# Performance work log

Hardware: AMD Instinct MI355X
Metric: run time of the kernel (lower is better)

## Reference

```python
import jax, jax.numpy as jnp
import numpy as np
from jax import lax

V, D, H = 32000, 512, 512  # vocab, embedding_dim, hidden_size (must match for the DxD matmul chain)
B, T, A = 64, 256, 4       # batch, sentence len, aspect len
EPS = 1e-5


def setup_inputs() -> dict:
    key = jax.random.key(0)
    ks = jax.random.split(key, 12)
    sc = 0.05
    return {
        "x": jax.random.randint(ks[0], (B, T), 0, V),
        "s": jax.random.randint(ks[1], (B, A), 0, V),
        "embed": jax.random.normal(ks[2], (V, D), jnp.float32) * sc,
        "W_ih": jax.random.normal(ks[3], (4 * H, D), jnp.float32) * sc,
        "W_hh": jax.random.normal(ks[4], (4 * H, H), jnp.float32) * sc,
        "b_lstm": jax.random.normal(ks[5], (4 * H,), jnp.float32) * sc,
        "w_y": jax.random.normal(ks[6], (D, D), jnp.float32) * sc,
        "w_t": jax.random.normal(ks[7], (D, D), jnp.float32) * sc,
        "w_p": jax.random.normal(ks[8], (D, D), jnp.float32) * sc,
        "w_x": jax.random.normal(ks[9], (D, D), jnp.float32) * sc,
        "w_f": jax.random.normal(ks[10], (D, D), jnp.float32) * sc,
        "b_f": jax.random.normal(ks[11], (D,), jnp.float32) * sc,
    }


def _lstm(emb, W_ih, W_hh, b):
    # emb: [B, T, D] -> hidden states [B, T, H]; PyTorch gate order i,f,g,o
    Bx = emb.shape[0]
    Hh = W_hh.shape[1]
    h0 = jnp.zeros((Bx, Hh), emb.dtype)
    c0 = jnp.zeros((Bx, Hh), emb.dtype)

    def step(carry, x_t):
        h, c = carry
        z = x_t @ W_ih.T + h @ W_hh.T + b  # [B, 4H]
        i, f, g, o = jnp.split(z, 4, axis=-1)
        c = jax.nn.sigmoid(f) * c + jax.nn.sigmoid(i) * jnp.tanh(g)
        h = jax.nn.sigmoid(o) * jnp.tanh(c)
        return (h, c), h

    _, hs = lax.scan(step, (h0, c0), jnp.swapaxes(emb, 0, 1))
    return jnp.swapaxes(hs, 0, 1)  # [B, T, H]


def reference(x, s, embed, W_ih, W_hh, b_lstm, w_y, w_t, w_p, w_x, w_f, b_f):
    # 1) embed + LSTM over the sentence
    emb = embed[x]                      # [B, T, D]
    Hs = _lstm(emb, W_ih, W_hh, b_lstm)  # [B, T, H]

    # 2) aspect: embed, batch-normalize per feature, sum over aspect tokens
    s_emb = embed[s]                    # [B, A, D]
    mu = s_emb.mean(axis=(0, 1))
    var = s_emb.var(axis=(0, 1))
    s_norm = ((s_emb - mu) * lax.rsqrt(var + EPS)).sum(axis=1)  # [B, D]

    # 3) FFT circular correlation: m_t = ifft(fft(h_t) * conj(fft(s))).real
    Hf = jnp.fft.fft(Hs, axis=-1)                      # [B, T, D] complex
    Sf = jnp.conj(jnp.fft.fft(s_norm, axis=-1))        # [B, D]
    m = jnp.fft.ifft(Hf * Sf[:, None, :], axis=-1).real.astype(Hs.dtype)  # [B, T, D]

    # 4) attention chain
    Y = jnp.tanh(jnp.einsum('de,bte->btd', w_y, m))            # [B, T, D]
    alpha = jax.nn.softmax(jnp.einsum('de,bte->btd', w_t, Y), axis=1)  # softmax over time
    r = jnp.einsum('btd,btd->bd', alpha, Hs)                   # [B, D]
    h_star = jnp.tanh(r @ w_p.T + Hs[:, -1] @ w_x.T)           # [B, D]
    return jax.nn.softmax(h_star @ w_f.T + b_f, axis=-1)       # [B, D]
```

## Files before the change

kernel.cpp:

```cpp
#include <hip/hip_runtime.h>


typedef __bf16 bf16x8 __attribute__((ext_vector_type(8)));
typedef float f32x4 __attribute__((ext_vector_type(4)));

#define B_ 64
#define T_ 256
#define D_ 512
#define H4 2048

__device__ __forceinline__ unsigned short f2bf(float f) {
    unsigned u = __float_as_uint(f);
    u += 0x7fffu + ((u >> 16) & 1u);
    return (unsigned short)(u >> 16);
}
__device__ __forceinline__ float bf2f(unsigned short x) {
    return __uint_as_float(((unsigned)x) << 16);
}
__device__ __forceinline__ float bf2f_lo(unsigned u) { return __uint_as_float(u << 16); }
__device__ __forceinline__ float bf2f_hi(unsigned u) { return __uint_as_float(u & 0xffff0000u); }

__device__ __forceinline__ float frcp(float x) { return __builtin_amdgcn_rcpf(x); }
__device__ __forceinline__ float fast_sigmoid(float x) {
    return frcp(1.f + __expf(-x));
}
__device__ __forceinline__ float fast_tanh(float x) {
    return 1.f - 2.f * frcp(1.f + __expf(2.f * x));
}

__global__ __launch_bounds__(256)
void gemm_bt(const void* __restrict__ Abase, int a_f32,
             const int* __restrict__ gather_idx,
             const float* __restrict__ Bmat,
             const float* __restrict__ circ_src,
             const float* __restrict__ bias,
             unsigned short* __restrict__ outb,
             float* __restrict__ outf,
             int N, int K,
             long A_bstride, long out_bstride,
             int act)
{
    __shared__ __align__(16) unsigned short Asm[128 * 40];
    __shared__ __align__(16) unsigned short Bsm[128 * 40];

    const int bz = blockIdx.z;
    const int tile_n = blockIdx.x * 128;
    const int tile_m = blockIdx.y * 128;
    const int tid = threadIdx.x;
    const int lane = tid & 63;
    const int w = tid >> 6;
    const int wm = (w >> 1) * 64;
    const int wn = (w & 1) * 64;

    const int srow = tid >> 1;
    const int skc = (tid & 1) * 16;

    const float* arow_f = nullptr;
    const unsigned short* arow_h = nullptr;
    if (a_f32) {
        const float* Af = (const float*)Abase;
        if (gather_idx) arow_f = Af + (long)gather_idx[tile_m + srow] * K;
        else            arow_f = Af + (long)bz * A_bstride + (long)(tile_m + srow) * K;
    } else {
        arow_h = (const unsigned short*)Abase + (long)bz * A_bstride + (long)(tile_m + srow) * K;
    }
    const float* brow = nullptr;
    const float* csrc = nullptr;
    if (circ_src) csrc = circ_src + bz * 512;
    else brow = Bmat + (long)(tile_n + srow) * K;

    f32x4 zero4 = {0.f, 0.f, 0.f, 0.f};
    f32x4 acc[4][4];
    #pragma unroll
    for (int mi = 0; mi < 4; mi++)
        #pragma unroll
        for (int ni = 0; ni < 4; ni++) acc[mi][ni] = zero4;

    const int fr = lane & 15;
    const int fq = (lane >> 4) * 8;

    for (int kc = 0; kc < K; kc += 32) {
        __syncthreads();
        if (a_f32) {
            float4 u0 = *(const float4*)(arow_f + kc + skc);
            float4 u1 = *(const float4*)(arow_f + kc + skc + 4);
            float4 u2 = *(const float4*)(arow_f + kc + skc + 8);
            float4 u3 = *(const float4*)(arow_f + kc + skc + 12);
            unsigned short tmp[16] __attribute__((aligned(16)));
            tmp[0] = f2bf(u0.x); tmp[1] = f2bf(u0.y); tmp[2]  = f2bf(u0.z); tmp[3]  = f2bf(u0.w);
            tmp[4] = f2bf(u1.x); tmp[5] = f2bf(u1.y); tmp[6]  = f2bf(u1.z); tmp[7]  = f2bf(u1.w);
            tmp[8] = f2bf(u2.x); tmp[9] = f2bf(u2.y); tmp[10] = f2bf(u2.z); tmp[11] = f2bf(u2.w);
            tmp[12] = f2bf(u3.x); tmp[13] = f2bf(u3.y); tmp[14] = f2bf(u3.z); tmp[15] = f2bf(u3.w);
            *(uint4*)&Asm[srow * 40 + skc]     = *(const uint4*)tmp;
            *(uint4*)&Asm[srow * 40 + skc + 8] = *(const uint4*)(tmp + 8);
        } else {
            *(uint4*)&Asm[srow * 40 + skc]     = *(const uint4*)(arow_h + kc + skc);
            *(uint4*)&Asm[srow * 40 + skc + 8] = *(const uint4*)(arow_h + kc + skc + 8);
        }
        if (csrc) {
            unsigned short tmp[16] __attribute__((aligned(16)));
            int n_abs = tile_n + srow;
            #pragma unroll
            for (int j = 0; j < 16; j++) {
                int k_abs = kc + skc + j;
                tmp[j] = f2bf(csrc[(k_abs - n_abs) & 511]);
            }
            *(uint4*)&Bsm[srow * 40 + skc]     = *(const uint4*)tmp;
            *(uint4*)&Bsm[srow * 40 + skc + 8] = *(const uint4*)(tmp + 8);
        } else {
            float4 u0 = *(const float4*)(brow + kc + skc);
            float4 u1 = *(const float4*)(brow + kc + skc + 4);
            float4 u2 = *(const float4*)(brow + kc + skc + 8);
            float4 u3 = *(const float4*)(brow + kc + skc + 12);
            unsigned short tmp[16] __attribute__((aligned(16)));
            tmp[0] = f2bf(u0.x); tmp[1] = f2bf(u0.y); tmp[2]  = f2bf(u0.z); tmp[3]  = f2bf(u0.w);
            tmp[4] = f2bf(u1.x); tmp[5] = f2bf(u1.y); tmp[6]  = f2bf(u1.z); tmp[7]  = f2bf(u1.w);
            tmp[8] = f2bf(u2.x); tmp[9] = f2bf(u2.y); tmp[10] = f2bf(u2.z); tmp[11] = f2bf(u2.w);
            tmp[12] = f2bf(u3.x); tmp[13] = f2bf(u3.y); tmp[14] = f2bf(u3.z); tmp[15] = f2bf(u3.w);
            *(uint4*)&Bsm[srow * 40 + skc]     = *(const uint4*)tmp;
            *(uint4*)&Bsm[srow * 40 + skc + 8] = *(const uint4*)(tmp + 8);
        }
        __syncthreads();
        bf16x8 av[4], bv[4];
        #pragma unroll
        for (int mi = 0; mi < 4; mi++)
            av[mi] = *(const bf16x8*)&Asm[(wm + mi * 16 + fr) * 40 + fq];
        #pragma unroll
        for (int ni = 0; ni < 4; ni++)
            bv[ni] = *(const bf16x8*)&Bsm[(wn + ni * 16 + fr) * 40 + fq];
        #pragma unroll
        for (int mi = 0; mi < 4; mi++)
            #pragma unroll
            for (int ni = 0; ni < 4; ni++)
                acc[mi][ni] = __builtin_amdgcn_mfma_f32_16x16x32_bf16(
                    av[mi], bv[ni], acc[mi][ni], 0, 0, 0);
    }

    #pragma unroll
    for (int mi = 0; mi < 4; mi++) {
        #pragma unroll
        for (int ni = 0; ni < 4; ni++) {
            #pragma unroll
            for (int rg = 0; rg < 4; rg++) {
                int row = tile_m + wm + mi * 16 + (lane >> 4) * 4 + rg;
                int col = tile_n + wn + ni * 16 + (lane & 15);
                float v = acc[mi][ni][rg];
                if (bias) v += bias[col];
                if (act == 1) v = fast_tanh(v);
                long oidx = (long)bz * out_bstride + (long)row * N + col;
                if (outb) outb[oidx] = f2bf(v);
                else outf[oidx] = v;
            }
        }
    }
}

#define WSTRIDE 520
#define SENT 0xFFFFFFFFu
#define ZL(g,r,d) zl[((g)*8+(r))*65+(d)]

__global__ __launch_bounds__(512, 2)
void persistent_lstm(const float* __restrict__ Whh,
                     const unsigned short* __restrict__ Zx,
                     unsigned int* __restrict__ Hsu)
{
    __shared__ __align__(16) unsigned short hsm[16 * WSTRIDE];
    __shared__ float zl[4 * 8 * 65];

    const int cq  = blockIdx.x & 7;
    const int nbp = blockIdx.x >> 3;
    const int tid = threadIdx.x;
    const int w = tid >> 6;
    const int lane = tid & 63;
    const int fr = lane & 15;
    const int fq = (lane >> 4) * 8;
    const int g = w >> 1;
    const int f = w & 1;

    bf16x8 wfrag[2][16];
    #pragma unroll
    for (int n = 0; n < 2; n++) {
        const float* wrow = Whh + (long)(g * 512 + nbp * 64 + f * 32 + n * 16 + fr) * 512;
        #pragma unroll
        for (int c = 0; c < 16; c++) {
            int k0 = c * 32 + fq;
            float4 u0 = *(const float4*)(wrow + k0);
            float4 u1 = *(const float4*)(wrow + k0 + 4);
            unsigned short tmp[8] __attribute__((aligned(16)));
            tmp[0] = f2bf(u0.x); tmp[1] = f2bf(u0.y); tmp[2] = f2bf(u0.z); tmp[3] = f2bf(u0.w);
            tmp[4] = f2bf(u1.x); tmp[5] = f2bf(u1.y); tmp[6] = f2bf(u1.z); tmp[7] = f2bf(u1.w);
            wfrag[n][c] = *(const bf16x8*)tmp;
        }
    }

    for (int i = tid; i < 16 * WSTRIDE / 2; i += 512)
        ((unsigned*)hsm)[i] = 0;

    int st_r[4], st_dp[4];
    #pragma unroll
    for (int k = 0; k < 4; k++) {
        int idx = k * 512 + tid;
        st_r[k] = idx >> 8;
        st_dp[k] = idx & 255;
    }

    const int grow = (tid & 255) >> 5;
    const int d0 = (tid & 31) * 2;
    const int b_own = cq * 8 + grow;
    const int dg = nbp * 64 + d0;
    float ca = 0.f, cb = 0.f;

    f32x4 zero4 = {0.f, 0.f, 0.f, 0.f};

    for (int t = 0; t < T_; t++) {
        unsigned zi_u = 0, zf_u = 0, zg_u = 0, zo_u = 0;
        if (tid < 256) {
            const long zb = ((long)b_own * T_ + t) * H4 + dg;
            zi_u = *(const unsigned*)&Zx[zb + 0 * 512];
            zf_u = *(const unsigned*)&Zx[zb + 1 * 512];
            zg_u = *(const unsigned*)&Zx[zb + 2 * 512];
            zo_u = *(const unsigned*)&Zx[zb + 3 * 512];
        }

        f32x4 an0 = zero4, an1 = zero4;
        if (t > 0) {
            unsigned vv[4];
            long ad[4];
            #pragma unroll
            for (int k = 0; k < 4; k++) {
                ad[k] = ((long)(cq * 8 + st_r[k]) * T_ + (t - 1)) * 256 + st_dp[k];
                vv[k] = __hip_atomic_load(Hsu + ad[k], __ATOMIC_RELAXED,
                                          __HIP_MEMORY_SCOPE_AGENT);
            }
            while (true) {
                bool pend = false;
                #pragma unroll
                for (int k = 0; k < 4; k++) pend |= (vv[k] == SENT);
                if (!__ballot(pend)) break;
                #pragma unroll
                for (int k = 0; k < 4; k++) {
                    vv[k] = __hip_atomic_load(Hsu + ad[k], __ATOMIC_RELAXED,
                                              __HIP_MEMORY_SCOPE_AGENT);
                }
            }
            #pragma unroll
            for (int k = 0; k < 4; k++) {
                *(unsigned*)&hsm[st_r[k] * WSTRIDE + st_dp[k] * 2] = vv[k];
            }
            __syncthreads();
            const unsigned short* arow = hsm + fr * WSTRIDE;
            f32x4 a0[4] = {zero4, zero4, zero4, zero4};
            f32x4 a1[4] = {zero4, zero4, zero4, zero4};
            #pragma unroll
            for (int c = 0; c < 16; c += 4) {
                bf16x8 x0 = *(const bf16x8*)(arow + (c + 0) * 32 + fq);
                bf16x8 x1 = *(const bf16x8*)(arow + (c + 1) * 32 + fq);
                bf16x8 x2 = *(const bf16x8*)(arow + (c + 2) * 32 + fq);
                bf16x8 x3 = *(const bf16x8*)(arow + (c + 3) * 32 + fq);
                a0[0] = __builtin_amdgcn_mfma_f32_16x16x32_bf16(x0, wfrag[0][c + 0], a0[0], 0, 0, 0);
                a0[1] = __builtin_amdgcn_mfma_f32_16x16x32_bf16(x1, wfrag[0][c + 1], a0[1], 0, 0, 0);
                a0[2] = __builtin_amdgcn_mfma_f32_16x16x32_bf16(x2, wfrag[0][c + 2], a0[2], 0, 0, 0);
                a0[3] = __builtin_amdgcn_mfma_f32_16x16x32_bf16(x3, wfrag[0][c + 3], a0[3], 0, 0, 0);
                a1[0] = __builtin_amdgcn_mfma_f32_16x16x32_bf16(x0, wfrag[1][c + 0], a1[0], 0, 0, 0);
                a1[1] = __builtin_amdgcn_mfma_f32_16x16x32_bf16(x1, wfrag[1][c + 1], a1[1], 0, 0, 0);
                a1[2] = __builtin_amdgcn_mfma_f32_16x16x32_bf16(x2, wfrag[1][c + 2], a1[2], 0, 0, 0);
                a1[3] = __builtin_amdgcn_mfma_f32_16x16x32_bf16(x3, wfrag[1][c + 3], a1[3], 0, 0, 0);
            }
            an0 = (a0[0] + a0[1]) + (a0[2] + a0[3]);
            an1 = (a1[0] + a1[1]) + (a1[2] + a1[3]);
        }
        if (lane < 32) {
            const int rb = (lane >> 4) * 4;
            const int cl = f * 32 + (lane & 15);
            #pragma unroll
            for (int rg = 0; rg < 4; rg++) {
                ZL(g, rb + rg, cl)      = an0[rg];
                ZL(g, rb + rg, cl + 16) = an1[rg];
            }
        }
        __syncthreads();
        if (tid < 256) {
            float zi0 = ZL(0, grow, d0)     + bf2f_lo(zi_u);
            float zi1 = ZL(0, grow, d0 + 1) + bf2f_hi(zi_u);
            float zf0 = ZL(1, grow, d0)     + bf2f_lo(zf_u);
            float zf1 = ZL(1, grow, d0 + 1) + bf2f_hi(zf_u);
            float zg0 = ZL(2, grow, d0)     + bf2f_lo(zg_u);
            float zg1 = ZL(2, grow, d0 + 1) + bf2f_hi(zg_u);
            float zo0 = ZL(3, grow, d0)     + bf2f_lo(zo_u);
            float zo1 = ZL(3, grow, d0 + 1) + bf2f_hi(zo_u);

            ca = fast_sigmoid(zf0) * ca + fast_sigmoid(zi0) * fast_tanh(zg0);
            cb = fast_sigmoid(zf1) * cb + fast_sigmoid(zi1) * fast_tanh(zg1);
            float h0 = fast_sigmoid(zo0) * fast_tanh(ca);
            float h1 = fast_sigmoid(zo1) * fast_tanh(cb);

            unsigned hp = (unsigned)f2bf(h0) | ((unsigned)f2bf(h1) << 16);
            __hip_atomic_store(Hsu + ((long)b_own * T_ + t) * 256 + nbp * 32 + (tid & 31),
                               hp, __ATOMIC_RELAXED, __HIP_MEMORY_SCOPE_AGENT);
        }
    }
}

__global__ __launch_bounds__(64)
void aspect_norm(const int* __restrict__ s,
                 const float* __restrict__ embed,
                 float* __restrict__ s_norm)
{
    __shared__ int sidx[256];
    const int tid = threadIdx.x;
    const int d = blockIdx.x * 64 + tid;
    for (int i = tid; i < 256; i += 64) sidx[i] = s[i];
    __syncthreads();
    float sum = 0.f, sq = 0.f;
    for (int i = 0; i < 256; i++) {
        float v = embed[(long)sidx[i] * D_ + d];
        sum += v; sq += v * v;
    }
    float mu = sum * (1.f / 256.f);
    float var = sq * (1.f / 256.f) - mu * mu;
    float rstd = rsqrtf(var + 1e-5f);
    for (int b = 0; b < 64; b++) {
        float acc = 0.f;
        #pragma unroll
        for (int a = 0; a < 4; a++) {
            acc += embed[(long)sidx[b * 4 + a] * D_ + d] - mu;
        }
        s_norm[b * D_ + d] = acc * rstd;
    }
}

__global__ __launch_bounds__(256)
void attn_r(const float* __restrict__ apre,
            const unsigned short* __restrict__ Hs,
            float* __restrict__ r)
{
    const int b = blockIdx.y;
    const int d = blockIdx.x * 256 + threadIdx.x;
    const float* ap = apre + (long)b * T_ * D_ + d;
    const unsigned short* hp = Hs + (long)b * T_ * D_ + d;
    float mx = ap[0], sm = 1.f;
    for (int t = 1; t < T_; t++) {
        float v = ap[(long)t * D_];
        if (v > mx) { sm = sm * __expf(mx - v) + 1.f; mx = v; }
        else sm += __expf(v - mx);
    }
    float acc = 0.f;
    for (int t = 0; t < T_; t++) {
        acc += __expf(ap[(long)t * D_] - mx) * bf2f(hp[(long)t * D_]);
    }
    r[b * D_ + d] = acc / sm;
}

__global__ __launch_bounds__(256)
void hstar_kernel(const float* __restrict__ r,
                  const unsigned short* __restrict__ Hs,
                  const float* __restrict__ w_p,
                  const float* __restrict__ w_x,
                  float* __restrict__ h_star)
{
    __shared__ float rs[512];
    __shared__ float hts[512];
    const int b = blockIdx.x, tid = threadIdx.x;
    const long hlast = ((long)b * T_ + (T_ - 1)) * D_;
    rs[tid] = r[b * D_ + tid];
    rs[tid + 256] = r[b * D_ + 256 + tid];
    hts[tid] = bf2f(Hs[hlast + tid]);
    hts[tid + 256] = bf2f(Hs[hlast + 256 + tid]);
    __syncthreads();
    for (int d = tid; d < 512; d += 256) {
        const float* wp = w_p + (long)d * D_;
        const float* wx = w_x + (long)d * D_;
        float acc = 0.f;
        for (int e = 0; e < 512; e += 4) {
            float4 p1 = *(const float4*)(wp + e);
            float4 p2 = *(const float4*)(wx + e);
            acc += p1.x * rs[e] + p1.y * rs[e + 1] + p1.z * rs[e + 2] + p1.w * rs[e + 3];
            acc += p2.x * hts[e] + p2.y * hts[e + 1] + p2.z * hts[e + 2] + p2.w * hts[e + 3];
        }
        h_star[b * D_ + d] = fast_tanh(acc);
    }
}

__global__ __launch_bounds__(256)
void out_kernel(const float* __restrict__ h_star,
                const float* __restrict__ w_f,
                const float* __restrict__ b_f,
                float* __restrict__ out)
{
    __shared__ float hs[512];
    __shared__ float lg[512];
    __shared__ float red[8];
    const int b = blockIdx.x, tid = threadIdx.x;
    hs[tid] = h_star[b * D_ + tid];
    hs[tid + 256] = h_star[b * D_ + 256 + tid];
    __syncthreads();
    for (int d = tid; d < 512; d += 256) {
        const float* wr = w_f + (long)d * D_;
        float acc = b_f[d];
        for (int e = 0; e < 512; e += 4) {
            float4 p = *(const float4*)(wr + e);
            acc += p.x * hs[e] + p.y * hs[e + 1] + p.z * hs[e + 2] + p.w * hs[e + 3];
        }
        lg[d] = acc;
    }
    __syncthreads();
    float m0 = fmaxf(lg[tid], lg[tid + 256]);
    for (int off = 32; off > 0; off >>= 1) m0 = fmaxf(m0, __shfl_down(m0, off, 64));
    if ((tid & 63) == 0) red[tid >> 6] = m0;
    __syncthreads();
    float bmax = fmaxf(fmaxf(red[0], red[1]), fmaxf(red[2], red[3]));
    float e0 = __expf(lg[tid] - bmax);
    float e1 = __expf(lg[tid + 256] - bmax);
    float s0 = e0 + e1;
    for (int off = 32; off > 0; off >>= 1) s0 += __shfl_down(s0, off, 64);
    if ((tid & 63) == 0) red[4 + (tid >> 6)] = s0;
    __syncthreads();
    float inv = 1.f / (red[4] + red[5] + red[6] + red[7]);
    out[b * D_ + tid] = e0 * inv;
    out[b * D_ + 256 + tid] = e1 * inv;
}

extern "C" void kernel_launch(void* const* d_in, const int* in_sizes, int n_in,
                              void* d_out, int out_size, void* d_ws, size_t ws_size,
                              hipStream_t stream)
{
    (void)in_sizes; (void)n_in; (void)out_size; (void)ws_size;

    const int* x = (const int*)d_in[0];
    const int* s = (const int*)d_in[1];
    const float* embed  = (const float*)d_in[2];
    const float* W_ih   = (const float*)d_in[3];
    const float* W_hh   = (const float*)d_in[4];
    const float* b_lstm = (const float*)d_in[5];
    const float* w_y = (const float*)d_in[6];
    const float* w_t = (const float*)d_in[7];
    const float* w_p = (const float*)d_in[8];
    const float* w_x = (const float*)d_in[9];
    const float* w_f = (const float*)d_in[10];
    const float* b_f = (const float*)d_in[11];

    char* ws = (char*)d_ws;
    unsigned short* Zx   = (unsigned short*)(ws + 0);
    float*          apre = (float*)(ws + 0);
    unsigned short* mbuf = (unsigned short*)(ws + 33554432);
    unsigned short* Ybuf = (unsigned short*)(ws + 50331648);
    unsigned short* Hs   = (unsigned short*)(ws + 67108864);
    float* s_norm = (float*)(ws + 86114304);
    float* rbuf   = (float*)(ws + 86245376);
    float* hstar  = (float*)(ws + 86376448);

    hipMemsetAsync(Hs, 0xFF, (size_t)B_ * T_ * D_ * 2, stream);

    aspect_norm<<<dim3(8), dim3(64), 0, stream>>>(s, embed, s_norm);

    gemm_bt<<<dim3(16, 128, 1), dim3(256), 0, stream>>>(
        embed, 1, x, W_ih, nullptr, b_lstm, Zx, nullptr,
        2048, 512, 0L, 0L, 0);

    persistent_lstm<<<dim3(64), dim3(512), 0, stream>>>(
        W_hh, Zx, (unsigned int*)Hs);


    gemm_bt<<<dim3(4, 2, 64), dim3(256), 0, stream>>>(
        Hs, 0, nullptr, nullptr, s_norm, nullptr, mbuf, nullptr,
        512, 512, (long)(T_ * D_), (long)(T_ * D_), 0);

    gemm_bt<<<dim3(4, 128, 1), dim3(256), 0, stream>>>(
        mbuf, 0, nullptr, w_y, nullptr, nullptr, Ybuf, nullptr,
        512, 512, 0L, 0L, 1);

    gemm_bt<<<dim3(4, 128, 1), dim3(256), 0, stream>>>(
        Ybuf, 0, nullptr, w_t, nullptr, nullptr, nullptr, apre,
        512, 512, 0L, 0L, 0);

    attn_r<<<dim3(2, 64), dim3(256), 0, stream>>>(apre, Hs, rbuf);

    hstar_kernel<<<dim3(64), dim3(256), 0, stream>>>(rbuf, Hs, w_p, w_x, hstar);

    out_kernel<<<dim3(64), dim3(256), 0, stream>>>(hstar, w_f, b_f, (float*)d_out);
}
```

Measured before the change: 1.043 ms.

## Halve persistent LSTM block to 256 threads, each wave computing one full gate

Each block of the persistent LSTM kernel now runs 4 waves instead of 8. Each wave holds the W_hh fragments for a whole gate (64 columns, 4 N-tiles) in registers, and all 256 threads take part in the elementwise cell update. This removes idle threads and cuts barrier and LDS coordination per timestep, since fewer waves sync. The cost is double the weight registers per wave and twice as many polling loads per thread, which lengthens the serial MFMA chain per wave.

```diff
diff --git a/kernel.cpp b/kernel.cpp
--- a/kernel.cpp
+++ b/kernel.cpp
@@ -159,7 +159,7 @@
 #define SENT 0xFFFFFFFFu
 #define ZL(g,r,d) zl[((g)*8+(r))*65+(d)]
 
-__global__ __launch_bounds__(512, 2)
+__global__ __launch_bounds__(256, 1)
 void persistent_lstm(const float* __restrict__ Whh,
                      const unsigned short* __restrict__ Zx,
                      unsigned int* __restrict__ Hsu)
@@ -174,13 +174,11 @@
     const int lane = tid & 63;
     const int fr = lane & 15;
     const int fq = (lane >> 4) * 8;
-    const int g = w >> 1;
-    const int f = w & 1;
-
-    bf16x8 wfrag[2][16];
+
+    bf16x8 wfrag[4][16];
     #pragma unroll
-    for (int n = 0; n < 2; n++) {
-        const float* wrow = Whh + (long)(g * 512 + nbp * 64 + f * 32 + n * 16 + fr) * 512;
+    for (int n = 0; n < 4; n++) {
+        const float* wrow = Whh + (long)(w * 512 + nbp * 64 + n * 16 + fr) * 512;
         #pragma unroll
         for (int c = 0; c < 16; c++) {
             int k0 = c * 32 + fq;
@@ -193,18 +191,18 @@
         }
     }
 
-    for (int i = tid; i < 16 * WSTRIDE / 2; i += 512)
+    for (int i = tid; i < 16 * WSTRIDE / 2; i += 256)
         ((unsigned*)hsm)[i] = 0;
 
-    int st_r[4], st_dp[4];
+    int st_r[8], st_dp[8];
     #pragma unroll
-    for (int k = 0; k < 4; k++) {
-        int idx = k * 512 + tid;
+    for (int k = 0; k < 8; k++) {
+        int idx = k * 256 + tid;
         st_r[k] = idx >> 8;
         st_dp[k] = idx & 255;
     }
 
-    const int grow = (tid & 255) >> 5;
+    const int grow = tid >> 5;
     const int d0 = (tid & 31) * 2;
     const int b_own = cq * 8 + grow;
     const int dg = nbp * 64 + d0;
@@ -213,8 +211,8 @@
     f32x4 zero4 = {0.f, 0.f, 0.f, 0.f};
 
     for (int t = 0; t < T_; t++) {
-        unsigned zi_u = 0, zf_u = 0, zg_u = 0, zo_u = 0;
-        if (tid < 256) {
+        unsigned zi_u, zf_u, zg_u, zo_u;
+        {
             const long zb = ((long)b_own * T_ + t) * H4 + dg;
             zi_u = *(const unsigned*)&Zx[zb + 0 * 512];
             zf_u = *(const unsigned*)&Zx[zb + 1 * 512];
@@ -222,12 +220,12 @@
             zo_u = *(const unsigned*)&Zx[zb + 3 * 512];
         }
 
-        f32x4 an0 = zero4, an1 = zero4;
+        f32x4 an[4] = {zero4, zero4, zero4, zero4};
         if (t > 0) {
-            unsigned vv[4];
-            long ad[4];
-            #pragma unroll
-            for (int k = 0; k < 4; k++) {
+            unsigned vv[8];
+            long ad[8];
+            #pragma unroll
+            for (int k = 0; k < 8; k++) {
                 ad[k] = ((long)(cq * 8 + st_r[k]) * T_ + (t - 1)) * 256 + st_dp[k];
                 vv[k] = __hip_atomic_load(Hsu + ad[k], __ATOMIC_RELAXED,
                                           __HIP_MEMORY_SCOPE_AGENT);
@@ -235,51 +233,49 @@
             while (true) {
                 bool pend = false;
                 #pragma unroll
-                for (int k = 0; k < 4; k++) pend |= (vv[k] == SENT);
+                for (int k = 0; k < 8; k++) pend |= (vv[k] == SENT);
                 if (!__ballot(pend)) break;
                 #pragma unroll
-                for (int k = 0; k < 4; k++) {
+                for (int k = 0; k < 8; k++) {
                     vv[k] = __hip_atomic_load(Hsu + ad[k], __ATOMIC_RELAXED,
                                               __HIP_MEMORY_SCOPE_AGENT);
                 }
             }
             #pragma unroll
-            for (int k = 0; k < 4; k++) {
+            for (int k = 0; k < 8; k++) {
                 *(unsigned*)&hsm[st_r[k] * WSTRIDE + st_dp[k] * 2] = vv[k];
             }
             __syncthreads();
             const unsigned short* arow = hsm + fr * WSTRIDE;
-            f32x4 a0[4] = {zero4, zero4, zero4, zero4};
-            f32x4 a1[4] = {zero4, zero4, zero4, zero4};
-            #pragma unroll
-            for (int c = 0; c < 16; c += 4) {
+            f32x4 acf[4][2];
+            #pragma unroll
+            for (int n = 0; n < 4; n++) { acf[n][0] = zero4; acf[n][1] = zero4; }
+            #pragma unroll
+            for (int c = 0; c < 16; c += 2) {
                 bf16x8 x0 = *(const bf16x8*)(arow + (c + 0) * 32 + fq);
                 bf16x8 x1 = *(const bf16x8*)(arow + (c + 1) * 32 + fq);
-                bf16x8 x2 = *(const bf16x8*)(arow + (c + 2) * 32 + fq);
-                bf16x8 x3 = *(const bf16x8*)(arow + (c + 3) * 32 + fq);
-                a0[0] = __builtin_amdgcn_mfma_f32_16x16x32_bf16(x0, wfrag[0][c + 0], a0[0], 0, 0, 0);
-                a0[1] = __builtin_amdgcn_mfma_f32_16x16x32_bf16(x1, wfrag[0][c + 1], a0[1], 0, 0, 0);
-                a0[2] = __builtin_amdgcn_mfma_f32_16x16x32_bf16(x2, wfrag[0][c + 2], a0[2], 0, 0, 0);
-                a0[3] = __builtin_amdgcn_mfma_f32_16x16x32_bf16(x3, wfrag[0][c + 3], a0[3], 0, 0, 0);
-                a1[0] = __builtin_amdgcn_mfma_f32_16x16x32_bf16(x0, wfrag[1][c + 0], a1[0], 0, 0, 0);
-                a1[1] = __builtin_amdgcn_mfma_f32_16x16x32_bf16(x1, wfrag[1][c + 1], a1[1], 0, 0, 0);
-                a1[2] = __builtin_amdgcn_mfma_f32_16x16x32_bf16(x2, wfrag[1][c + 2], a1[2], 0, 0, 0);
-                a1[3] = __builtin_amdgcn_mfma_f32_16x16x32_bf16(x3, wfrag[1][c + 3], a1[3], 0, 0, 0);
-            }
-            an0 = (a0[0] + a0[1]) + (a0[2] + a0[3]);
-            an1 = (a1[0] + a1[1]) + (a1[2] + a1[3]);
+                #pragma unroll
+                for (int n = 0; n < 4; n++) {
+                    acf[n][0] = __builtin_amdgcn_mfma_f32_16x16x32_bf16(x0, wfrag[n][c + 0], acf[n][0], 0, 0, 0);
+                    acf[n][1] = __builtin_amdgcn_mfma_f32_16x16x32_bf16(x1, wfrag[n][c + 1], acf[n][1], 0, 0, 0);
+                }
+            }
+            #pragma unroll
+            for (int n = 0; n < 4; n++) an[n] = acf[n][0] + acf[n][1];
         }
         if (lane < 32) {
             const int rb = (lane >> 4) * 4;
-            const int cl = f * 32 + (lane & 15);
-            #pragma unroll
-            for (int rg = 0; rg < 4; rg++) {
-                ZL(g, rb + rg, cl)      = an0[rg];
-                ZL(g, rb + rg, cl + 16) = an1[rg];
+            const int cl = lane & 15;
+            #pragma unroll
+            for (int n = 0; n < 4; n++) {
+                #pragma unroll
+                for (int rg = 0; rg < 4; rg++) {
+                    ZL(w, rb + rg, n * 16 + cl) = an[n][rg];
+                }
             }
         }
         __syncthreads();
-        if (tid < 256) {
+        {
             float zi0 = ZL(0, grow, d0)     + bf2f_lo(zi_u);
             float zi1 = ZL(0, grow, d0 + 1) + bf2f_hi(zi_u);
             float zf0 = ZL(1, grow, d0)     + bf2f_lo(zf_u);
@@ -457,7 +453,7 @@
         embed, 1, x, W_ih, nullptr, b_lstm, Zx, nullptr,
         2048, 512, 0L, 0L, 0);
 
-    persistent_lstm<<<dim3(64), dim3(512), 0, stream>>>(
+    persistent_lstm<<<dim3(64), dim3(256), 0, stream>>>(
         W_hh, Zx, (unsigned int*)Hs);
 
 
```

Result: slower. 1.177 ms (+12.9%).
